# Performance work log

Measured on AMD Instinct MI355X. Metric: run time of the kernel, lower is better.

The kernel has to match this reference:

```python
import jax, jax.numpy as jnp
import numpy as np

WS = 7          # window size
SHIFT = WS // 2 # shift for odd blocks
NH = 8          # num heads
EPS = 1e-5


def _rel_pos_index(ws):
    coords = np.stack(np.meshgrid(np.arange(ws), np.arange(ws), indexing='ij'))  # (2, ws, ws)
    cf = coords.reshape(2, -1)                                  # (2, N)
    rc = (cf[:, :, None] - cf[:, None, :]).transpose(1, 2, 0)   # (N, N, 2)
    rc[..., 0] += ws - 1
    rc[..., 1] += ws - 1
    rc[..., 0] *= 2 * ws - 1
    return rc.sum(-1)  # (N, N) int


def _attn_mask(Hp, Wp, ws, shift):
    # (nW, N, N) additive mask with 0 / -100, as in the torch code
    img = np.zeros((Hp, Wp), dtype=np.float32)
    cnt = 0
    slices = (slice(0, -ws), slice(-ws, -shift), slice(-shift, None))
    for h in slices:
        for w in slices:
            img[h, w] = cnt
            cnt += 1
    mw = img.reshape(Hp // ws, ws, Wp // ws, ws).transpose(0, 2, 1, 3).reshape(-1, ws * ws)
    am = mw[:, None, :] - mw[:, :, None]
    return np.where(am != 0, -100.0, 0.0).astype(np.float32)


def _layernorm(x, w, b):
    m = x.mean(-1, keepdims=True)
    v = ((x - m) ** 2).mean(-1, keepdims=True)
    return (x - m) * jax.lax.rsqrt(v + EPS) * w + b


def _window_partition(x, ws):
    B, H, W, C = x.shape
    x = x.reshape(B, H // ws, ws, W // ws, ws, C).transpose(0, 1, 3, 2, 4, 5)
    return x.reshape(-1, ws * ws, C)


def _window_reverse(w, ws, H, W):
    B = w.shape[0] // (H // ws * W // ws)
    x = w.reshape(B, H // ws, W // ws, ws, ws, -1).transpose(0, 1, 3, 2, 4, 5)
    return x.reshape(B, H, W, -1)


def _window_msa(xw, qkv_w, qkv_b, proj_w, proj_b, rpb, rel_idx, mask):
    Bw, N, C = xw.shape
    hd = C // NH
    qkv = (xw @ qkv_w.T + qkv_b).reshape(Bw, N, 3, NH, hd).transpose(2, 0, 3, 1, 4)
    q, k, v = qkv[0] * (hd ** -0.5), qkv[1], qkv[2]
    attn = jnp.einsum('bhnd,bhmd->bhnm', q, k)                      # (Bw, NH, N, N)
    bias = rpb[rel_idx.reshape(-1)].reshape(N, N, NH).transpose(2, 0, 1)
    attn = attn + bias[None]
    if mask is not None:
        nW = mask.shape[0]
        attn = attn.reshape(Bw // nW, nW, NH, N, N) + mask[None, :, None]
        attn = attn.reshape(Bw, NH, N, N)
    attn = jax.nn.softmax(attn, axis=-1)
    out = jnp.einsum('bhnm,bhmd->bhnd', attn, v).transpose(0, 2, 1, 3).reshape(Bw, N, C)
    return out @ proj_w.T + proj_b


def _forward(x, ln1_w, ln1_b, qkv_w, qkv_b, proj_w, proj_b, rpb,
             ln2_w, ln2_b, mlp_w1, mlp_b1, mlp_w2, mlp_b2, H, W):
    B, L, C = x.shape
    rel_idx = _rel_pos_index(WS)
    pad_r = (WS - W % WS) % WS
    pad_b = (WS - H % WS) % WS
    Hp, Wp = H + pad_b, W + pad_r
    depth = ln1_w.shape[0]
    for i in range(depth):
        shift = 0 if i % 2 == 0 else SHIFT
        shortcut = x
        h = _layernorm(x, ln1_w[i], ln1_b[i]).reshape(B, H, W, C)
        if pad_r > 0 or pad_b > 0:
            h = jnp.pad(h, ((0, 0), (0, pad_b), (0, pad_r), (0, 0)))
        if shift > 0:
            h = jnp.roll(h, (-shift, -shift), axis=(1, 2))
            mask = jnp.asarray(_attn_mask(Hp, Wp, WS, shift))
        else:
            mask = None
        hw = _window_partition(h, WS)
        hw = _window_msa(hw, qkv_w[i], qkv_b[i], proj_w[i], proj_b[i], rpb[i], rel_idx, mask)
        h = _window_reverse(hw.reshape(-1, WS, WS, C), WS, Hp, Wp)
        if shift > 0:
            h = jnp.roll(h, (shift, shift), axis=(1, 2))
        if pad_r > 0 or pad_b > 0:
            h = h[:, :H, :W, :]
        x = shortcut + h.reshape(B, H * W, C)
        m = _layernorm(x, ln2_w[i], ln2_b[i])
        m = jax.nn.gelu(m @ mlp_w1[i].T + mlp_b1[i], approximate=False)
        x = x + (m @ mlp_w2[i].T + mlp_b2[i])
    return x


def setup_inputs() -> dict:
    key = jax.random.key(0)
    ks = jax.random.split(key, 8)
    B, H, W, C, D = 8, 112, 112, 256, 2
    hid = 4 * C
    return {
        'x': jax.random.normal(ks[0], (B, H * W, C), jnp.float32),
        'ln1_w': jnp.ones((D, C), jnp.float32),
        'ln1_b': jnp.zeros((D, C), jnp.float32),
        'qkv_w': jax.random.normal(ks[1], (D, 3 * C, C), jnp.float32) * 0.02,
        'qkv_b': jnp.zeros((D, 3 * C), jnp.float32),
        'proj_w': jax.random.normal(ks[2], (D, C, C), jnp.float32) * 0.02,
        'proj_b': jnp.zeros((D, C), jnp.float32),
        'rpb': jax.random.normal(ks[3], (D, (2 * WS - 1) ** 2, NH), jnp.float32) * 0.02,
        'ln2_w': jnp.ones((D, C), jnp.float32),
        'ln2_b': jnp.zeros((D, C), jnp.float32),
        'mlp_w1': jax.random.normal(ks[4], (D, hid, C), jnp.float32) * 0.02,
        'mlp_b1': jnp.zeros((D, hid), jnp.float32),
        'mlp_w2': jax.random.normal(ks[5], (D, C, hid), jnp.float32) * 0.02,
        'mlp_b2': jnp.zeros((D, C), jnp.float32),
        'H': H,
        'W': W,
    }


def reference(x, ln1_w, ln1_b, qkv_w, qkv_b, proj_w, proj_b, rpb,
              ln2_w, ln2_b, mlp_w1, mlp_b1, mlp_w2, mlp_b2, H, W):
    return _forward(x, ln1_w, ln1_b, qkv_w, qkv_b, proj_w, proj_b, rpb,
                    ln2_w, ln2_b, mlp_w1, mlp_b1, mlp_w2, mlp_b2, H, W)
```

## Files before the change

### kernel.cpp

```cpp
#include <hip/hip_runtime.h>

typedef unsigned short u16;
typedef unsigned int u32;
typedef __attribute__((ext_vector_type(8))) short bf16x8;
typedef __attribute__((ext_vector_type(4))) float f32x4;
typedef __attribute__((ext_vector_type(16))) float f32x16;
typedef __attribute__((ext_vector_type(8))) unsigned short u16x8;
typedef const __attribute__((address_space(1))) void gvoid;
typedef __attribute__((address_space(3))) void svoid;

#define T_TOK 100352
#define CDIM 256
#define ATTN_SCALE 0.17677669529663687f

__device__ __forceinline__ u16 f2bf(float f) {
    u32 u = __float_as_uint(f);
    u32 r = (u + 0x7fffu + ((u >> 16) & 1u)) >> 16;
    return (u16)r;
}
__device__ __forceinline__ float bf2f(u16 h) {
    return __uint_as_float(((u32)h) << 16);
}
__device__ __forceinline__ u32 cvtpk(float lo, float hi) {
    u32 r;
    asm("v_cvt_pk_bf16_f32 %0, %1, %2" : "=v"(r) : "v"(lo), "v"(hi));
    return r;
}
__device__ __forceinline__ float gelu_f(float x) {
    float z = 0.7978845608028654f * (x + 0.044715f * x * x * x);
    float e = __expf(2.0f * z);
    float th = 1.0f - 2.0f * __builtin_amdgcn_rcpf(e + 1.0f);
    return 0.5f * x * (1.0f + th);
}
__device__ __forceinline__ int div7(int q) { return (q * 37) >> 8; }
__device__ __forceinline__ int reg3(int r) { return r < 105 ? 0 : (r < 109 ? 1 : 2); }

__global__ void cvt_kernel(const float* __restrict__ in, u16* __restrict__ out, int n) {
    int i = blockIdx.x * 256 + threadIdx.x;
    if (i < n) out[i] = f2bf(in[i]);
}

__global__ void cvt_w1_kernel(const float* __restrict__ in, u16* __restrict__ out) {
    int idx = blockIdx.x * 256 + threadIdx.x;
    int e = idx & 7, r = (idx >> 3) & 31, g = (idx >> 8) & 31;
    int ch = (idx >> 13) & 31, L = idx >> 18;
    out[idx] = f2bf(in[(size_t)L*262144 + (ch*32 + r)*256 + g*8 + e]);
}
__global__ void cvt_w2_kernel(const float* __restrict__ in, u16* __restrict__ out) {
    int idx = blockIdx.x * 256 + threadIdx.x;
    int e = idx & 7, r = (idx >> 3) & 255, g = (idx >> 11) & 3;
    int ch = (idx >> 13) & 31, L = idx >> 18;
    out[idx] = f2bf(in[(size_t)L*262144 + r*1024 + ch*32 + g*8 + e]);
}

__global__ __launch_bounds__(256) void ln_kernel(
    const float* __restrict__ X, const float* __restrict__ w,
    const float* __restrict__ b, u16* __restrict__ Y)
{
    int wid = threadIdx.x >> 6, l = threadIdx.x & 63;
    int t = blockIdx.x * 4 + wid;
    const float4 x4 = ((const float4*)(X + (size_t)t * CDIM))[l];
    float s  = x4.x + x4.y + x4.z + x4.w;
    float s2 = x4.x*x4.x + x4.y*x4.y + x4.z*x4.z + x4.w*x4.w;
    #pragma unroll
    for (int o = 32; o; o >>= 1) { s += __shfl_xor(s, o); s2 += __shfl_xor(s2, o); }
    float mean = s * (1.0f/256.0f);
    float var  = s2 * (1.0f/256.0f) - mean*mean;
    float rstd = rsqrtf(var + 1e-5f);
    float4 w4 = ((const float4*)w)[l];
    float4 b4 = ((const float4*)b)[l];
    ushort4 o4;
    o4.x = f2bf((x4.x - mean)*rstd*w4.x + b4.x);
    o4.y = f2bf((x4.y - mean)*rstd*w4.y + b4.y);
    o4.z = f2bf((x4.z - mean)*rstd*w4.z + b4.z);
    o4.w = f2bf((x4.w - mean)*rstd*w4.w + b4.w);
    ((ushort4*)(Y + (size_t)t * CDIM))[l] = o4;
}

template<int EPI>
__global__ __launch_bounds__(256) void gemm_kernel(
    const u16* __restrict__ A, const u16* __restrict__ Bw,
    const float* __restrict__ bias, void* __restrict__ outp,
    const float* __restrict__ res, int N, int K, int nTn)
{
    __shared__ __align__(16) char lds_raw[69632];
    u16 (*lds)[2][128 * 64] = (u16(*)[2][128 * 64])lds_raw;
    const int tid = threadIdx.x;
    const int l = tid & 63;
    const int w = tid >> 6;
    const int wr = w >> 1, wc = w & 1;

    const int nBlocks = gridDim.x;
    const int cpx = nBlocks >> 3;
    const int lin = (blockIdx.x & 7) * cpx + (blockIdx.x >> 3);
    const int nT = lin % nTn;
    const int mT = lin / nTn;

    f32x4 acc[4][4];
    #pragma unroll
    for (int m = 0; m < 4; ++m)
        #pragma unroll
        for (int n = 0; n < 4; ++n) acc[m][n] = (f32x4){0.f,0.f,0.f,0.f};

    const int sr = tid >> 3;
    const int sg = tid & 7;

    #define STAGE(buf, kt)                                                              \
        {                                                                               \
            _Pragma("unroll")                                                           \
            for (int c = 0; c < 4; ++c) {                                               \
                int r = c*32 + sr;                                                      \
                int gsrc = sg ^ (r & 7);                                                \
                const u16* ga = A  + (size_t)(mT*128 + r) * K + (kt) + gsrc*8;          \
                const u16* gb = Bw + (size_t)(nT*128 + r) * K + (kt) + gsrc*8;          \
                u16* la = &lds[buf][0][(c*256 + w*64) * 8];                              \
                u16* lb = &lds[buf][1][(c*256 + w*64) * 8];                              \
                __builtin_amdgcn_global_load_lds((gvoid*)ga, (svoid*)la, 16, 0, 0);     \
                __builtin_amdgcn_global_load_lds((gvoid*)gb, (svoid*)lb, 16, 0, 0);     \
            }                                                                           \
        }

    const int nSteps = K >> 6;
    int cur = 0;

    STAGE(0, 0);
    asm volatile("s_waitcnt vmcnt(0)" ::: "memory");
    __builtin_amdgcn_s_barrier();
    asm volatile("" ::: "memory");

    const int lr = l & 15, gq = l >> 4;
    for (int t = 0; t < nSteps; ++t) {
        bf16x8 a[2][4], b[2][4];
        #pragma unroll
        for (int kk = 0; kk < 2; ++kk) {
            #pragma unroll
            for (int m = 0; m < 4; ++m) {
                int r = wr*64 + m*16 + lr;
                int g = kk*4 + gq;
                a[kk][m] = *(const bf16x8*)&lds[cur][0][r*64 + (g ^ (r & 7))*8];
            }
            #pragma unroll
            for (int n = 0; n < 4; ++n) {
                int r = wc*64 + n*16 + lr;
                int g = kk*4 + gq;
                b[kk][n] = *(const bf16x8*)&lds[cur][1][r*64 + (g ^ (r & 7))*8];
            }
        }
        if (t + 1 < nSteps) STAGE(cur ^ 1, (t + 1) * 64);

        __builtin_amdgcn_s_setprio(1);
        #pragma unroll
        for (int kk = 0; kk < 2; ++kk)
            #pragma unroll
            for (int m = 0; m < 4; ++m)
                #pragma unroll
                for (int n = 0; n < 4; ++n)
                    acc[m][n] = __builtin_amdgcn_mfma_f32_16x16x32_bf16(a[kk][m], b[kk][n], acc[m][n], 0, 0, 0);
        __builtin_amdgcn_s_setprio(0);

        asm volatile("s_waitcnt vmcnt(0)" ::: "memory");
        __builtin_amdgcn_s_barrier();
        asm volatile("" ::: "memory");
        cur ^= 1;
    }
    #undef STAGE

    if (EPI == 2) {
        float* epf = (float*)lds_raw + w * (64 * 68);
        #pragma unroll
        for (int m = 0; m < 4; ++m)
            #pragma unroll
            for (int n = 0; n < 4; ++n) {
                float bb = bias[nT*128 + wc*64 + n*16 + lr];
                #pragma unroll
                for (int j = 0; j < 4; ++j)
                    epf[(m*16 + gq*4 + j)*68 + n*16 + lr] = acc[m][n][j] + bb;
            }
        const int rr4 = l >> 4, cc4 = (l & 15) * 4;
        float* outf = (float*)outp;
        #pragma unroll
        for (int p = 0; p < 16; ++p) {
            float4 vv = *(const float4*)&epf[(p*4 + rr4)*68 + cc4];
            size_t grow = (size_t)(mT*128 + wr*64 + p*4 + rr4);
            size_t gcol = (size_t)(nT*128 + wc*64 + cc4);
            float4 rv = *(const float4*)(res + grow*N + gcol);
            float4 ov; ov.x = vv.x + rv.x; ov.y = vv.y + rv.y;
            ov.z = vv.z + rv.z; ov.w = vv.w + rv.w;
            *(float4*)(outf + grow*N + gcol) = ov;
        }
    } else {
        float* epf = (float*)lds_raw + w * (64 * 68);
        #pragma unroll
        for (int m = 0; m < 4; ++m)
            #pragma unroll
            for (int n = 0; n < 4; ++n) {
                float bb = bias[nT*128 + wc*64 + n*16 + lr];
                #pragma unroll
                for (int j = 0; j < 4; ++j) {
                    float v = acc[m][n][j] + bb;
                    if (EPI == 1) v = gelu_f(v);
                    epf[(m*16 + gq*4 + j)*68 + n*16 + lr] = v;
                }
            }
        const int rr8 = l >> 3, cc8 = (l & 7) * 8;
        u16* outw = (u16*)outp;
        #pragma unroll
        for (int p = 0; p < 8; ++p) {
            float4 v0 = *(const float4*)&epf[(p*8 + rr8)*68 + cc8];
            float4 v1 = *(const float4*)&epf[(p*8 + rr8)*68 + cc8 + 4];
            union { u32 u[4]; u16x8 v; } pk;
            pk.u[0] = cvtpk(v0.x, v0.y); pk.u[1] = cvtpk(v0.z, v0.w);
            pk.u[2] = cvtpk(v1.x, v1.y); pk.u[3] = cvtpk(v1.z, v1.w);
            size_t grow = (size_t)(mT*128 + wr*64 + p*8 + rr8);
            size_t gcol = (size_t)(nT*128 + wc*64 + cc8);
            *(u16x8*)(outw + grow*N + gcol) = pk.v;
        }
    }
}

__global__ __launch_bounds__(256, 2) void mlp_kernel(
    const u16* __restrict__ Y, const u16* __restrict__ W1t,
    const float* __restrict__ B1, const u16* __restrict__ W2t,
    const float* __restrict__ B2, const float* __restrict__ res,
    float* __restrict__ xout)
{
    __shared__ __align__(16) char lds_raw[69632];

    const int tid = threadIdx.x;
    const int l = tid & 63;
    const int w = tid >> 6;
    const int lo = l & 31;
    const int hi = l >> 5;
    const int row0 = blockIdx.x * 128 + w * 32;

    bf16x8 yf[16];
    #pragma unroll
    for (int kt = 0; kt < 16; ++kt)
        yf[kt] = *(const bf16x8*)(Y + (size_t)(row0 + lo) * 256 + kt*16 + hi*8);

    float b2v[8];
    #pragma unroll
    for (int ot = 0; ot < 8; ++ot) b2v[ot] = B2[ot*32 + lo];

    ((float4*)(lds_raw + 65536))[tid] = ((const float4*)B1)[tid];

    f32x16 acc[8];
    #pragma unroll
    for (int ot = 0; ot < 8; ++ot) {
        f32x16 z;
        #pragma unroll
        for (int i = 0; i < 16; ++i) z[i] = 0.f;
        acc[ot] = z;
    }

    #define MSTG(buf, ch)                                                                  \
        {                                                                                  \
            _Pragma("unroll")                                                              \
            for (int c = 0; c < 4; ++c) {                                                  \
                const u16* g1 = W1t + (size_t)(ch)*8192 + (c*256 + tid)*8;                 \
                u16* d1 = (u16*)(lds_raw + (buf)*32768 + (c*256 + w*64)*16);               \
                __builtin_amdgcn_global_load_lds((gvoid*)g1, (svoid*)d1, 16, 0, 0);        \
                const u16* g2 = W2t + (size_t)(ch)*8192 + (c*256 + tid)*8;                 \
                u16* d2 = (u16*)(lds_raw + (buf)*32768 + 16384 + (c*256 + w*64)*16);       \
                __builtin_amdgcn_global_load_lds((gvoid*)g2, (svoid*)d2, 16, 0, 0);        \
            }                                                                              \
        }

    MSTG(0, 0);
    asm volatile("s_waitcnt vmcnt(0)" ::: "memory");
    __builtin_amdgcn_s_barrier();
    asm volatile("" ::: "memory");

    #pragma unroll 1
    for (int ch = 0; ch < 32; ++ch) {
        const int cur = ch & 1;
        const char* w1b = lds_raw + cur*32768;
        const char* w2b = w1b + 16384;

        if (ch + 1 < 32) MSTG(cur ^ 1, ch + 1);

        f32x16 ht0, ht1;
        #pragma unroll
        for (int i = 0; i < 16; ++i) { ht0[i] = 0.f; ht1[i] = 0.f; }
        #pragma unroll
        for (int kt = 0; kt < 16; kt += 2) {
            bf16x8 w1f0 = *(const bf16x8*)(w1b + (2*kt + hi)*512 + lo*16);
            bf16x8 w1f1 = *(const bf16x8*)(w1b + (2*kt + 2 + hi)*512 + lo*16);
            ht0 = __builtin_amdgcn_mfma_f32_32x32x16_bf16(w1f0, yf[kt], ht0, 0, 0, 0);
            ht1 = __builtin_amdgcn_mfma_f32_32x32x16_bf16(w1f1, yf[kt+1], ht1, 0, 0, 0);
        }

        const float* b1l = (const float*)(lds_raw + 65536) + ch*32;
        f32x16 ht;
        #pragma unroll
        for (int i = 0; i < 16; ++i) {
            int r = (i & 3) + 8*(i >> 2) + 4*hi;
            ht[i] = gelu_f(ht0[i] + ht1[i] + b1l[r]);
        }

        u32 pk[8];
        #pragma unroll
        for (int j = 0; j < 8; ++j) pk[j] = cvtpk(ht[2*j], ht[2*j+1]);
        bf16x8 pa[2];
        #pragma unroll
        for (int s2 = 0; s2 < 2; ++s2) {
            u32 a0 = pk[s2*4 + 0], a1 = pk[s2*4 + 1];
            u32 a2 = pk[s2*4 + 2], a3 = pk[s2*4 + 3];
            asm volatile("v_permlane32_swap_b32 %0, %1" : "+v"(a0), "+v"(a2));
            asm volatile("v_permlane32_swap_b32 %0, %1" : "+v"(a1), "+v"(a3));
            union { u32 u[4]; bf16x8 v; } pf;
            pf.u[0] = a0; pf.u[1] = a1; pf.u[2] = a2; pf.u[3] = a3;
            pa[s2] = pf.v;
        }

        __builtin_amdgcn_s_setprio(1);
        #pragma unroll
        for (int ot = 0; ot < 8; ++ot) {
            #pragma unroll
            for (int ks = 0; ks < 2; ++ks) {
                bf16x8 w2f = *(const bf16x8*)(w2b + (2*ks + hi)*4096 + (ot*32 + lo)*16);
                acc[ot] = __builtin_amdgcn_mfma_f32_32x32x16_bf16(pa[ks], w2f, acc[ot], 0, 0, 0);
            }
        }
        __builtin_amdgcn_s_setprio(0);

        asm volatile("s_waitcnt vmcnt(0)" ::: "memory");
        __builtin_amdgcn_s_barrier();
        asm volatile("" ::: "memory");
    }
    #undef MSTG

    float* scr = (float*)(lds_raw + w * 16640);
    #pragma unroll 1
    for (int half = 0; half < 2; ++half) {
        #pragma unroll
        for (int ot4 = 0; ot4 < 4; ++ot4) {
            int ot = half*4 + ot4;
            #pragma unroll
            for (int i = 0; i < 16; ++i) {
                int r = (i & 3) + 8*(i >> 2) + 4*hi;
                scr[r*130 + ot4*32 + lo] = acc[ot][i] + b2v[ot];
            }
        }
        asm volatile("s_waitcnt lgkmcnt(0)" ::: "memory");
        __builtin_amdgcn_sched_barrier(0);
        const int rr = l >> 5, cc = (l & 31) * 4;
        #pragma unroll
        for (int p = 0; p < 16; ++p) {
            float4 vv = *(const float4*)&scr[(p*2 + rr)*130 + cc];
            size_t off = (size_t)(row0 + p*2 + rr) * 256 + half*128 + cc;
            float4 rv = *(const float4*)(res + off);
            float4 ov; ov.x = vv.x + rv.x; ov.y = vv.y + rv.y;
            ov.z = vv.z + rv.z; ov.w = vv.w + rv.w;
            *(float4*)(xout + off) = ov;
        }
        asm volatile("s_waitcnt lgkmcnt(0)" ::: "memory");
        __builtin_amdgcn_sched_barrier(0);
    }
}

__global__ __launch_bounds__(256) void attn_kernel(
    const u16* __restrict__ qkv, const float* __restrict__ rpb,
    u16* __restrict__ outb, int shift)
{
    __shared__ u16 Vt[8][2048];
    __shared__ float biasl[8 * 176];
    __shared__ int tok[64];

    const int t = threadIdx.x;
    const int w = t >> 6;
    const int l = t & 63;
    const int lo = l & 31;
    const int hi = l >> 5;
    const int win = blockIdx.x;
    const int wj = win & 15, wi = (win >> 4) & 15, bb = win >> 8;

    if (t < 64) {
        int qq = t > 48 ? 48 : t;
        int i = div7(qq), j = qq - i*7;
        int rr = wi*7 + i + shift; if (rr >= 112) rr -= 112;
        int cc = wj*7 + j + shift; if (cc >= 112) cc -= 112;
        tok[t] = bb*12544 + rr*112 + cc;
    }
    for (int i2 = t; i2 < 1352; i2 += 256)
        biasl[(i2 & 7)*176 + (i2 >> 3)] = rpb[i2];
    __syncthreads();

    int iqv[2], jqv[2], regq[2];
    #pragma unroll
    for (int nt = 0; nt < 2; ++nt) {
        int q = nt*32 + lo; int qb = q > 48 ? 48 : q;
        int iq = div7(qb), jq = qb - iq*7;
        iqv[nt] = iq; jqv[nt] = jq;
        regq[nt] = 0;
        if (shift > 0) regq[nt] = reg3(wi*7 + iq)*3 + reg3(wj*7 + jq);
    }

    #pragma unroll 1
    for (int hh = 0; hh < 2; ++hh) {
        const int h = 2*w + hh;

        {
            u16x8 vreg[4];
            if (l < 49) {
                const u16x8* vs = (const u16x8*)(qkv + (size_t)tok[l]*768 + 512 + h*32);
                #pragma unroll
                for (int c4 = 0; c4 < 4; ++c4) vreg[c4] = vs[c4];
            } else {
                #pragma unroll
                for (int c4 = 0; c4 < 4; ++c4) vreg[c4] = (u16x8){0,0,0,0,0,0,0,0};
            }
            u16* vt = &Vt[h][0];
            #pragma unroll
            for (int c4 = 0; c4 < 4; ++c4)
                #pragma unroll
                for (int e = 0; e < 8; ++e)
                    vt[(c4*8 + e)*64 + (l ^ (e << 3))] = vreg[c4][e];
        }

        bf16x8 kf[2][2], qf[2][2];
        #pragma unroll
        for (int mt = 0; mt < 2; ++mt)
            #pragma unroll
            for (int td = 0; td < 2; ++td)
                kf[mt][td] = *(const bf16x8*)(qkv + (size_t)tok[mt*32 + lo]*768 + 256 + h*32 + td*16 + hi*8);
        #pragma unroll
        for (int nt = 0; nt < 2; ++nt)
            #pragma unroll
            for (int td = 0; td < 2; ++td)
                qf[nt][td] = *(const bf16x8*)(qkv + (size_t)tok[nt*32 + lo]*768 + h*32 + td*16 + hi*8);

        f32x16 s[2][2];
        #pragma unroll
        for (int mt = 0; mt < 2; ++mt)
            #pragma unroll
            for (int nt = 0; nt < 2; ++nt) {
                f32x16 z;
                #pragma unroll
                for (int i = 0; i < 16; ++i) z[i] = 0.f;
                s[mt][nt] = z;
            }
        #pragma unroll
        for (int td = 0; td < 2; ++td)
            #pragma unroll
            for (int mt = 0; mt < 2; ++mt)
                #pragma unroll
                for (int nt = 0; nt < 2; ++nt)
                    s[mt][nt] = __builtin_amdgcn_mfma_f32_32x32x16_bf16(kf[mt][td], qf[nt][td], s[mt][nt], 0, 0, 0);

        asm volatile("s_waitcnt lgkmcnt(0)" ::: "memory");
        __builtin_amdgcn_sched_barrier(0);

        const float* bh = biasl + h*176;
        #pragma unroll
        for (int mt = 0; mt < 2; ++mt) {
            #pragma unroll
            for (int i = 0; i < 16; ++i) {
                int r = (i & 3) + 8*(i >> 2) + 4*hi;
                int k = mt*32 + r;
                bool valid = k < 49;
                int kb = valid ? k : 48;
                int ik = div7(kb), jk = kb - ik*7;
                int regk = 0;
                if (shift > 0) regk = reg3(wi*7 + ik)*3 + reg3(wj*7 + jk);
                #pragma unroll
                for (int nt = 0; nt < 2; ++nt) {
                    float v = s[mt][nt][i] * ATTN_SCALE
                            + bh[(iqv[nt] - ik + 6)*13 + (jqv[nt] - jk + 6)];
                    if (shift > 0 && regq[nt] != regk) v -= 100.0f;
                    if (!valid) v = -1e30f;
                    s[mt][nt][i] = v;
                }
            }
        }

        #pragma unroll
        for (int nt = 0; nt < 2; ++nt) {
            float mx = -1e30f;
            #pragma unroll
            for (int i = 0; i < 16; ++i) mx = fmaxf(mx, fmaxf(s[0][nt][i], s[1][nt][i]));
            mx = fmaxf(mx, __shfl_xor(mx, 32));
            float sum = 0.f;
            #pragma unroll
            for (int mt = 0; mt < 2; ++mt)
                #pragma unroll
                for (int i = 0; i < 16; ++i) {
                    float e = __expf(s[mt][nt][i] - mx);
                    s[mt][nt][i] = e;
                    sum += e;
                }
            sum += __shfl_xor(sum, 32);
            float inv = __builtin_amdgcn_rcpf(sum);

            u32 pk[2][8];
            #pragma unroll
            for (int mt = 0; mt < 2; ++mt)
                #pragma unroll
                for (int j = 0; j < 8; ++j)
                    pk[mt][j] = (u32)f2bf(s[mt][nt][2*j] * inv)
                              | ((u32)f2bf(s[mt][nt][2*j + 1] * inv) << 16);

            f32x16 o;
            #pragma unroll
            for (int i = 0; i < 16; ++i) o[i] = 0.f;
            #pragma unroll
            for (int kt = 0; kt < 4; ++kt) {
                const int mt = kt >> 1;
                const int base = (kt & 1) * 4;
                u32 a0 = pk[mt][base + 0], a1 = pk[mt][base + 1];
                u32 a2 = pk[mt][base + 2], a3 = pk[mt][base + 3];
                asm volatile("v_permlane32_swap_b32 %0, %1" : "+v"(a0), "+v"(a2));
                asm volatile("v_permlane32_swap_b32 %0, %1" : "+v"(a1), "+v"(a3));
                union { u32 u[4]; bf16x8 v; } pf;
                pf.u[0] = a0; pf.u[1] = a1; pf.u[2] = a2; pf.u[3] = a3;
                bf16x8 vb = *(const bf16x8*)(&Vt[h][lo*64 + ((kt*16 + hi*8) ^ ((lo & 7) << 3))]);
                o = __builtin_amdgcn_mfma_f32_32x32x16_bf16(pf.v, vb, o, 0, 0, 0);
            }

            #pragma unroll
            for (int i = 0; i < 16; ++i) {
                int q = nt*32 + (i & 3) + 8*(i >> 2) + 4*hi;
                if (q < 49)
                    outb[(size_t)tok[q]*256 + h*32 + lo] = f2bf(o[i]);
            }
        }
    }
}

extern "C" void kernel_launch(void* const* d_in, const int* in_sizes, int n_in,
                              void* d_out, int out_size, void* d_ws, size_t ws_size,
                              hipStream_t stream) {
    const float* x_in   = (const float*)d_in[0];
    const float* ln1_w  = (const float*)d_in[1];
    const float* ln1_b  = (const float*)d_in[2];
    const float* qkv_w  = (const float*)d_in[3];
    const float* qkv_b  = (const float*)d_in[4];
    const float* proj_w = (const float*)d_in[5];
    const float* proj_b = (const float*)d_in[6];
    const float* rpb    = (const float*)d_in[7];
    const float* ln2_w  = (const float*)d_in[8];
    const float* ln2_b  = (const float*)d_in[9];
    const float* mlp_w1 = (const float*)d_in[10];
    const float* mlp_b1 = (const float*)d_in[11];
    const float* mlp_w2 = (const float*)d_in[12];
    const float* mlp_b2 = (const float*)d_in[13];
    float* xout = (float*)d_out;

    char* p = (char*)d_ws;
    u16* wq = (u16*)p;  p += (size_t)2*768*256*2;
    u16* wp = (u16*)p;  p += (size_t)2*256*256*2;
    u16* w1t = (u16*)p; p += (size_t)2*1024*256*2;
    u16* w2t = (u16*)p; p += (size_t)2*256*1024*2;
    u16* buf_y   = (u16*)p; p += (size_t)T_TOK*256*2;
    u16* buf_big = (u16*)p;

    {
        int n;
        n = 2*768*256;  cvt_kernel<<<(n+255)/256, 256, 0, stream>>>(qkv_w,  wq, n);
        n = 2*256*256;  cvt_kernel<<<(n+255)/256, 256, 0, stream>>>(proj_w, wp, n);
        cvt_w1_kernel<<<2048, 256, 0, stream>>>(mlp_w1, w1t);
        cvt_w2_kernel<<<2048, 256, 0, stream>>>(mlp_w2, w2t);
    }

    for (int i = 0; i < 2; ++i) {
        const int shift = (i == 0) ? 0 : 3;
        const float* xcur = (i == 0) ? x_in : xout;

        ln_kernel<<<T_TOK/4, 256, 0, stream>>>(xcur, ln1_w + i*256, ln1_b + i*256, buf_y);
        gemm_kernel<0><<<784*6, 256, 0, stream>>>(
            buf_y, wq + (size_t)i*768*256, qkv_b + i*768, buf_big, nullptr, 768, 256, 6);
        attn_kernel<<<2048, 256, 0, stream>>>(buf_big, rpb + i*169*8, buf_y, shift);
        gemm_kernel<2><<<784*2, 256, 0, stream>>>(
            buf_y, wp + (size_t)i*256*256, proj_b + i*256, xout, xcur, 256, 256, 2);
        ln_kernel<<<T_TOK/4, 256, 0, stream>>>(xout, ln2_w + i*256, ln2_b + i*256, buf_y);
        mlp_kernel<<<784, 256, 0, stream>>>(
            buf_y, w1t + (size_t)i*262144, mlp_b1 + i*1024,
            w2t + (size_t)i*262144, mlp_b2 + i*256, xout, xout);
    }
}
```

Measured before the change: 961.7 us.

## Load MLP weight fragments directly from global memory instead of LDS staging

The MLP kernel stops double-buffering W1/W2 chunks into LDS with global_load_lds and barriers. Each wave now reads its weight fragments straight from global memory, relying on L2/cache reuse across waves. This removes the per-chunk barrier and the LDS staging traffic, but every wave now issues redundant global loads and exposes their latency inside the MFMA loop. The B1 bias region in LDS is moved, and a __syncthreads is added before it is read.

```diff
diff --git a/kernel.cpp b/kernel.cpp
--- a/kernel.cpp
+++ b/kernel.cpp
@@ -224,7 +224,7 @@
     const float* __restrict__ B2, const float* __restrict__ res,
     float* __restrict__ xout)
 {
-    __shared__ __align__(16) char lds_raw[69632];
+    __shared__ __align__(16) char lds_raw[70656];
 
     const int tid = threadIdx.x;
     const int l = tid & 63;
@@ -242,7 +242,8 @@
     #pragma unroll
     for (int ot = 0; ot < 8; ++ot) b2v[ot] = B2[ot*32 + lo];
 
-    ((float4*)(lds_raw + 65536))[tid] = ((const float4*)B1)[tid];
+    ((float4*)(lds_raw + 66560))[tid] = ((const float4*)B1)[tid];
+    __syncthreads();
 
     f32x16 acc[8];
     #pragma unroll
@@ -253,44 +254,26 @@
         acc[ot] = z;
     }
 
-    #define MSTG(buf, ch)                                                                  \
-        {                                                                                  \
-            _Pragma("unroll")                                                              \
-            for (int c = 0; c < 4; ++c) {                                                  \
-                const u16* g1 = W1t + (size_t)(ch)*8192 + (c*256 + tid)*8;                 \
-                u16* d1 = (u16*)(lds_raw + (buf)*32768 + (c*256 + w*64)*16);               \
-                __builtin_amdgcn_global_load_lds((gvoid*)g1, (svoid*)d1, 16, 0, 0);        \
-                const u16* g2 = W2t + (size_t)(ch)*8192 + (c*256 + tid)*8;                 \
-                u16* d2 = (u16*)(lds_raw + (buf)*32768 + 16384 + (c*256 + w*64)*16);       \
-                __builtin_amdgcn_global_load_lds((gvoid*)g2, (svoid*)d2, 16, 0, 0);        \
-            }                                                                              \
-        }
-
-    MSTG(0, 0);
-    asm volatile("s_waitcnt vmcnt(0)" ::: "memory");
-    __builtin_amdgcn_s_barrier();
-    asm volatile("" ::: "memory");
+    const u16* w1base = W1t + hi*256 + lo*8;
+    const u16* w2base = W2t + hi*2048 + lo*8;
 
     #pragma unroll 1
     for (int ch = 0; ch < 32; ++ch) {
-        const int cur = ch & 1;
-        const char* w1b = lds_raw + cur*32768;
-        const char* w2b = w1b + 16384;
-
-        if (ch + 1 < 32) MSTG(cur ^ 1, ch + 1);
+        const u16* w1c = w1base + ch*8192;
+        const u16* w2c = w2base + ch*8192;
 
         f32x16 ht0, ht1;
         #pragma unroll
         for (int i = 0; i < 16; ++i) { ht0[i] = 0.f; ht1[i] = 0.f; }
         #pragma unroll
         for (int kt = 0; kt < 16; kt += 2) {
-            bf16x8 w1f0 = *(const bf16x8*)(w1b + (2*kt + hi)*512 + lo*16);
-            bf16x8 w1f1 = *(const bf16x8*)(w1b + (2*kt + 2 + hi)*512 + lo*16);
+            bf16x8 w1f0 = *(const bf16x8*)(w1c + kt*512);
+            bf16x8 w1f1 = *(const bf16x8*)(w1c + kt*512 + 512);
             ht0 = __builtin_amdgcn_mfma_f32_32x32x16_bf16(w1f0, yf[kt], ht0, 0, 0, 0);
             ht1 = __builtin_amdgcn_mfma_f32_32x32x16_bf16(w1f1, yf[kt+1], ht1, 0, 0, 0);
         }
 
-        const float* b1l = (const float*)(lds_raw + 65536) + ch*32;
+        const float* b1l = (const float*)(lds_raw + 66560) + ch*32;
         f32x16 ht;
         #pragma unroll
         for (int i = 0; i < 16; ++i) {
@@ -313,22 +296,15 @@
             pa[s2] = pf.v;
         }
 
-        __builtin_amdgcn_s_setprio(1);
         #pragma unroll
         for (int ot = 0; ot < 8; ++ot) {
             #pragma unroll
             for (int ks = 0; ks < 2; ++ks) {
-                bf16x8 w2f = *(const bf16x8*)(w2b + (2*ks + hi)*4096 + (ot*32 + lo)*16);
+                bf16x8 w2f = *(const bf16x8*)(w2c + ks*4096 + ot*256);
                 acc[ot] = __builtin_amdgcn_mfma_f32_32x32x16_bf16(pa[ks], w2f, acc[ot], 0, 0, 0);
             }
         }
-        __builtin_amdgcn_s_setprio(0);
-
-        asm volatile("s_waitcnt vmcnt(0)" ::: "memory");
-        __builtin_amdgcn_s_barrier();
-        asm volatile("" ::: "memory");
-    }
-    #undef MSTG
+    }
 
     float* scr = (float*)(lds_raw + w * 16640);
     #pragma unroll 1
```

Measured after the change: 1.343 ms. 1.4x slower.
